# Kernel tuning notes

Hardware: AMD Instinct MI355X
Metric: run time of the kernel (lower is better)

Reference implementation:

```python
import jax, jax.numpy as jnp
import numpy as np

B, S, DIN, DOUT, R, NL, T = 4, 4096, 1024, 1024, 16, 8, 4

def setup_inputs() -> dict:
    key = jax.random.key(0)
    k1, k2, k3, k4, k5 = jax.random.split(key, 5)
    return {
        "x": jax.random.normal(k1, (B, S, DIN), dtype=jnp.float32),
        "W": jax.random.normal(k2, (DOUT, DIN), dtype=jnp.float32) * 0.02,
        "bias": jax.random.normal(k3, (DOUT,), dtype=jnp.float32) * 0.02,
        "lora_A": jax.random.normal(k4, (NL, R, DIN), dtype=jnp.float32) * 0.02,
        "lora_B": jax.random.normal(k5, (NL, DOUT, R), dtype=jnp.float32) * 0.02,
        "tuner_index": jnp.arange(T, dtype=jnp.int64) if jax.config.jax_enable_x64 else jnp.arange(T, dtype=jnp.int32),
    }

def reference(x, W, bias, lora_A, lora_B, tuner_index):
    # Per adapter ti: F.linear(x, W + B_ti @ A_ti, bias)
    # == x @ W.T + (x @ A_ti.T) @ B_ti.T + bias  (fused low-rank form, same math)
    A = lora_A[tuner_index]   # [T, r, Din]
    Bm = lora_B[tuner_index]  # [T, Dout, r]
    base = jnp.einsum('bsd,od->bso', x, W) + bias          # [B, S, Dout]
    low = jnp.einsum('bsd,trd->tbsr', x, A)                # [T, B, S, r]
    delta = jnp.einsum('tbsr,tor->tbso', low, Bm)          # [T, B, S, Dout]
    return base[None, ...] + delta                         # [T, B, S, Dout]
```

## Files before the change

kernel.cpp:

```cpp
#include <hip/hip_runtime.h>


typedef __attribute__((ext_vector_type(8))) _Float16 f16x8;
typedef __attribute__((ext_vector_type(4))) float f32x4;
typedef __attribute__((ext_vector_type(4))) unsigned short us4;
typedef __attribute__((ext_vector_type(8))) unsigned short us8;

namespace {
constexpr int kM = 16384, kDin = 1024, kDout = 1024, kR = 16, kT = 4;
constexpr size_t OFF_XF  = 0;
constexpr size_t OFF_WF  = 33554432;
constexpr size_t OFF_LOW = 35651584;
}

__device__ inline unsigned short f2h(float f) {
  _Float16 h = (_Float16)f;
  return __builtin_bit_cast(unsigned short, h);
}
__device__ inline void gload_lds16(const void* g, void* l) {
  __builtin_amdgcn_global_load_lds(
      (const __attribute__((address_space(1))) unsigned int*)g,
      (__attribute__((address_space(3))) unsigned int*)l, 16, 0, 0);
}
__device__ inline f32x4 mfma_f16(f16x8 a, f16x8 b, f32x4 c) {
  return __builtin_amdgcn_mfma_f32_16x16x32_f16(a, b, c, 0, 0, 0);
}

__global__ __launch_bounds__(256) void cvt_W(const float* __restrict__ W,
                                             unsigned short* __restrict__ wf) {
  constexpr int NW4 = kDout * kDin / 4;
  const int stride = gridDim.x * blockDim.x;
  for (int j = blockIdx.x * blockDim.x + threadIdx.x; j < NW4; j += stride) {
    const float4 v = ((const float4*)W)[j];
    us4 h;
    h[0] = f2h(v.x); h[1] = f2h(v.y); h[2] = f2h(v.z); h[3] = f2h(v.w);
    ((us4*)wf)[j] = h;
  }
}

__global__ __launch_bounds__(256) void lora_low(const float* __restrict__ x,
                                                const float* __restrict__ A,
                                                const int* __restrict__ tuner,
                                                unsigned short* __restrict__ lowb,
                                                unsigned short* __restrict__ xf) {
  __shared__ float xs[64][34];
  __shared__ float as[64][66];
  const int tid = threadIdx.x;
  const int i0  = blockIdx.x * 32;
  const int tx  = tid & 15;
  const int ty  = tid >> 4;
  float acc[2][4] = {{0.f, 0.f, 0.f, 0.f}, {0.f, 0.f, 0.f, 0.f}};

  for (int kt = 0; kt < kDin; kt += 64) {
    __syncthreads();
#pragma unroll
    for (int p = 0; p < 2; ++p) {
      const int f = tid + p * 256;
      const int row = f >> 4, kq = (f & 15) * 4;
      const float4 v = *(const float4*)(x + (size_t)(i0 + row) * kDin + kt + kq);
      xs[kq + 0][row] = v.x; xs[kq + 1][row] = v.y;
      xs[kq + 2][row] = v.z; xs[kq + 3][row] = v.w;
      us4 h;
      h[0] = f2h(v.x); h[1] = f2h(v.y); h[2] = f2h(v.z); h[3] = f2h(v.w);
      *(us4*)(xf + (size_t)(i0 + row) * kDin + kt + kq) = h;
    }
#pragma unroll
    for (int p = 0; p < 4; ++p) {
      const int f = tid + p * 256;
      const int ar = f >> 4, kq = (f & 15) * 4;
      const int ti = tuner[ar >> 4];
      const float4 v = *(const float4*)(A + ((size_t)ti * kR + (ar & 15)) * kDin + kt + kq);
      as[kq + 0][ar] = v.x; as[kq + 1][ar] = v.y;
      as[kq + 2][ar] = v.z; as[kq + 3][ar] = v.w;
    }
    __syncthreads();
#pragma unroll 8
    for (int k = 0; k < 64; ++k) {
      const float a0 = xs[k][ty * 2], a1 = xs[k][ty * 2 + 1];
      const float b0 = as[k][tx * 4], b1 = as[k][tx * 4 + 1];
      const float b2 = as[k][tx * 4 + 2], b3 = as[k][tx * 4 + 3];
      acc[0][0] += a0 * b0; acc[0][1] += a0 * b1; acc[0][2] += a0 * b2; acc[0][3] += a0 * b3;
      acc[1][0] += a1 * b0; acc[1][1] += a1 * b1; acc[1][2] += a1 * b2; acc[1][3] += a1 * b3;
    }
  }
#pragma unroll
  for (int ii = 0; ii < 2; ++ii) {
    us4 o;
#pragma unroll
    for (int j = 0; j < 4; ++j) o[j] = f2h(acc[ii][j]);
    *(us4*)(lowb + ((size_t)(tx >> 2) * kM + i0 + ty * 2 + ii) * kR + (tx & 3) * 4) = o;
  }
}

__global__ __launch_bounds__(256) void lora_main(
    const unsigned short* __restrict__ xf, const unsigned short* __restrict__ wf,
    const float* __restrict__ bias, const float* __restrict__ Bm,
    const int* __restrict__ tuner, const unsigned short* __restrict__ lowb,
    float* __restrict__ out) {
  __shared__ __align__(16) unsigned char smem[32768];
  const int tid  = threadIdx.x;
  const int lane = tid & 63;
  const int w    = tid >> 6;

  const int swz = ((int)blockIdx.x & 7) * 128 + ((int)blockIdx.x >> 3);
  const int bm = swz >> 3, bn = swz & 7;
  const size_t i0 = (size_t)bm * 128, j0 = (size_t)bn * 128;
  const int wm = w >> 1, wn = w & 1;

  const int wp = w & 1;
  const unsigned short* gsrc = (w < 2) ? xf : wf;
  const size_t grow0 = ((w < 2) ? i0 : j0) + wp * 64;
  const unsigned short* gbase =
      gsrc + (grow0 + (lane >> 2)) * kDin + ((lane & 3) ^ ((lane >> 3) & 3)) * 8;
  const int stoff = (w >> 1) * 8192 + wp * 4096;

  f32x4 acc[4][4];
#pragma unroll
  for (int n = 0; n < 4; ++n)
#pragma unroll
    for (int m = 0; m < 4; ++m) acc[n][m] = (f32x4){0.f, 0.f, 0.f, 0.f};

  const int kg = lane >> 4;
  const int rl = lane & 15;
  const int csw = kg ^ ((rl >> 1) & 3);
  const int rdA = (wm * 64 + rl) * 64 + csw * 16;
  const int rdB = 8192 + (wn * 64 + rl) * 64 + csw * 16;

  auto compute_step = [&](const unsigned char* B0) {
    f16x8 a[4], b[4];
#pragma unroll
    for (int m = 0; m < 4; ++m) {
      a[m] = *(const f16x8*)(B0 + rdA + m * 1024);
      b[m] = *(const f16x8*)(B0 + rdB + m * 1024);
    }
    __builtin_amdgcn_s_setprio(1);
#pragma unroll
    for (int n = 0; n < 4; ++n)
#pragma unroll
      for (int m = 0; m < 4; ++m)
        acc[n][m] = mfma_f16(b[n], a[m], acc[n][m]);
    __builtin_amdgcn_s_setprio(0);
  };

  {
    unsigned char* dst = smem + stoff;
#pragma unroll
    for (int c = 0; c < 4; ++c)
      gload_lds16(gbase + c * 16 * kDin, dst + c * 1024);
  }

  for (int s = 0; s < 31; ++s) {
    const int p = s & 1;
    {
      unsigned char* dst = smem + (p ^ 1) * 16384 + stoff;
      const unsigned short* src = gbase + (s + 1) * 32;
#pragma unroll
      for (int c = 0; c < 4; ++c)
        gload_lds16(src + c * 16 * kDin, dst + c * 1024);
    }
    asm volatile("s_waitcnt vmcnt(4)" ::: "memory");
    __builtin_amdgcn_s_barrier();
    asm volatile("" ::: "memory");
    compute_step(smem + p * 16384);
    asm volatile("s_waitcnt lgkmcnt(0)" ::: "memory");
    __builtin_amdgcn_s_barrier();
    asm volatile("" ::: "memory");
  }
  asm volatile("s_waitcnt vmcnt(0)" ::: "memory");
  __builtin_amdgcn_s_barrier();
  asm volatile("" ::: "memory");
  compute_step(smem + 16384);

#pragma unroll
  for (int n = 0; n < 4; ++n) {
    const f32x4 bv = *(const f32x4*)(bias + j0 + wn * 64 + n * 16 + kg * 4);
#pragma unroll
    for (int m = 0; m < 4; ++m)
#pragma unroll
      for (int r = 0; r < 4; ++r) acc[n][m][r] += bv[r];
  }

  {
    unsigned char* p = (tid < 128) ? (smem + 4096 + tid * 32)
                                   : (smem + 12288 + (tid - 128) * 32);
    const us8 z = {0, 0, 0, 0, 0, 0, 0, 0};
    *(us8*)p = z;
    *(us8*)(p + 16) = z;
  }

  for (int t = 0; t < kT; ++t) {
    __syncthreads();
    {
      const int row = tid >> 1, half = tid & 1;
      const us8 lv = *(const us8*)(lowb + ((size_t)t * kM + i0 + row) * kR + half * 8);
      *(us8*)(smem + half * 2048 + row * 16) = lv;
      const int ti = tuner[t];
      const float* bp = Bm + ((size_t)ti * kDout + j0 + row) * kR + half * 8;
      const float4 m0 = *(const float4*)bp;
      const float4 m1 = *(const float4*)(bp + 4);
      us8 mv;
      mv[0] = f2h(m0.x); mv[1] = f2h(m0.y); mv[2] = f2h(m0.z); mv[3] = f2h(m0.w);
      mv[4] = f2h(m1.x); mv[5] = f2h(m1.y); mv[6] = f2h(m1.z); mv[7] = f2h(m1.w);
      *(us8*)(smem + 8192 + half * 2048 + row * 16) = mv;
    }
    __syncthreads();

    f16x8 lf[4], mf[4];
#pragma unroll
    for (int m = 0; m < 4; ++m)
      lf[m] = *(const f16x8*)(smem + kg * 2048 + (wm * 64 + m * 16 + rl) * 16);
#pragma unroll
    for (int n = 0; n < 4; ++n)
      mf[n] = *(const f16x8*)(smem + 8192 + kg * 2048 + (wn * 64 + n * 16 + rl) * 16);

#pragma unroll
    for (int n = 0; n < 4; ++n)
#pragma unroll
      for (int m = 0; m < 4; ++m) {
        const f32x4 d = mfma_f16(mf[n], lf[m], acc[n][m]);
        const size_t row = (size_t)t * kM + i0 + wm * 64 + m * 16 + rl;
        const int    col = (int)j0 + wn * 64 + n * 16 + kg * 4;
        *(f32x4*)(out + row * kDout + col) = d;
      }
  }
}

extern "C" void kernel_launch(void* const* d_in, const int* in_sizes, int n_in,
                              void* d_out, int out_size, void* d_ws, size_t ws_size,
                              hipStream_t stream) {
  const float* x    = (const float*)d_in[0];
  const float* W    = (const float*)d_in[1];
  const float* bias = (const float*)d_in[2];
  const float* lA   = (const float*)d_in[3];
  const float* lB   = (const float*)d_in[4];
  const int*   ti   = (const int*)d_in[5];
  float* out = (float*)d_out;

  unsigned char* ws = (unsigned char*)d_ws;
  unsigned short* xfp  = (unsigned short*)(ws + OFF_XF);
  unsigned short* wfp  = (unsigned short*)(ws + OFF_WF);
  unsigned short* lowb = (unsigned short*)(ws + OFF_LOW);

  cvt_W<<<64, 256, 0, stream>>>(W, wfp);
  lora_low<<<kM / 32, 256, 0, stream>>>(x, lA, ti, lowb, xfp);
  lora_main<<<1024, 256, 0, stream>>>(xfp, wfp, bias, lB, ti, lowb, out);
}
```

Before: 170.6 us.

## Fuse W conversion into lora_low, shrink main tile to 128x64, nontemporal stores

```diff
diff --git a/kernel.cpp b/kernel.cpp
--- a/kernel.cpp
+++ b/kernel.cpp
@@ -26,23 +26,25 @@
   return __builtin_amdgcn_mfma_f32_16x16x32_f16(a, b, c, 0, 0, 0);
 }
 
-__global__ __launch_bounds__(256) void cvt_W(const float* __restrict__ W,
-                                             unsigned short* __restrict__ wf) {
-  constexpr int NW4 = kDout * kDin / 4;
-  const int stride = gridDim.x * blockDim.x;
-  for (int j = blockIdx.x * blockDim.x + threadIdx.x; j < NW4; j += stride) {
-    const float4 v = ((const float4*)W)[j];
-    us4 h;
-    h[0] = f2h(v.x); h[1] = f2h(v.y); h[2] = f2h(v.z); h[3] = f2h(v.w);
-    ((us4*)wf)[j] = h;
-  }
-}
-
 __global__ __launch_bounds__(256) void lora_low(const float* __restrict__ x,
+                                                const float* __restrict__ W,
                                                 const float* __restrict__ A,
                                                 const int* __restrict__ tuner,
                                                 unsigned short* __restrict__ lowb,
-                                                unsigned short* __restrict__ xf) {
+                                                unsigned short* __restrict__ xf,
+                                                unsigned short* __restrict__ wf) {
+  {
+    const int idx = blockIdx.x * 256 + threadIdx.x;
+#pragma unroll
+    for (int p = 0; p < 2; ++p) {
+      const int j = idx + p * 131072;
+      const float4 v = ((const float4*)W)[j];
+      us4 h;
+      h[0] = f2h(v.x); h[1] = f2h(v.y); h[2] = f2h(v.z); h[3] = f2h(v.w);
+      ((us4*)wf)[j] = h;
+    }
+  }
+
   __shared__ float xs[64][34];
   __shared__ float as[64][66];
   const int tid = threadIdx.x;
@@ -97,26 +99,31 @@
     const float* __restrict__ bias, const float* __restrict__ Bm,
     const int* __restrict__ tuner, const unsigned short* __restrict__ lowb,
     float* __restrict__ out) {
-  __shared__ __align__(16) unsigned char smem[32768];
+  __shared__ __align__(16) unsigned char smem[24576];
   const int tid  = threadIdx.x;
   const int lane = tid & 63;
   const int w    = tid >> 6;
 
-  const int swz = ((int)blockIdx.x & 7) * 128 + ((int)blockIdx.x >> 3);
-  const int bm = swz >> 3, bn = swz & 7;
-  const size_t i0 = (size_t)bm * 128, j0 = (size_t)bn * 128;
+  const int swz = ((int)blockIdx.x & 7) * 256 + ((int)blockIdx.x >> 3);
+  const int bm = swz >> 4, bn = swz & 15;
+  const size_t i0 = (size_t)bm * 128, j0 = (size_t)bn * 64;
   const int wm = w >> 1, wn = w & 1;
 
-  const int wp = w & 1;
-  const unsigned short* gsrc = (w < 2) ? xf : wf;
-  const size_t grow0 = ((w < 2) ? i0 : j0) + wp * 64;
-  const unsigned short* gbase =
-      gsrc + (grow0 + (lane >> 2)) * kDin + ((lane & 3) ^ ((lane >> 3) & 3)) * 8;
-  const int stoff = (w >> 1) * 8192 + wp * 4096;
-
-  f32x4 acc[4][4];
-#pragma unroll
-  for (int n = 0; n < 4; ++n)
+  const int chsw = ((lane & 3) ^ ((lane >> 3) & 3)) * 8;
+  const unsigned short* gsrc_q[3];
+  int ldsoff_q[3];
+#pragma unroll
+  for (int q = 0; q < 3; ++q) {
+    const int c = 3 * w + q;
+    const bool isA = c < 8;
+    const size_t rowb = (isA ? i0 + c * 16 : j0 + (c - 8) * 16) + (lane >> 2);
+    gsrc_q[q] = (isA ? xf : wf) + rowb * kDin + chsw;
+    ldsoff_q[q] = c * 1024;
+  }
+
+  f32x4 acc[2][4];
+#pragma unroll
+  for (int n = 0; n < 2; ++n)
 #pragma unroll
     for (int m = 0; m < 4; ++m) acc[n][m] = (f32x4){0.f, 0.f, 0.f, 0.f};
 
@@ -124,44 +131,40 @@
   const int rl = lane & 15;
   const int csw = kg ^ ((rl >> 1) & 3);
   const int rdA = (wm * 64 + rl) * 64 + csw * 16;
-  const int rdB = 8192 + (wn * 64 + rl) * 64 + csw * 16;
+  const int rdB = 8192 + (wn * 32 + rl) * 64 + csw * 16;
 
   auto compute_step = [&](const unsigned char* B0) {
-    f16x8 a[4], b[4];
-#pragma unroll
-    for (int m = 0; m < 4; ++m) {
-      a[m] = *(const f16x8*)(B0 + rdA + m * 1024);
-      b[m] = *(const f16x8*)(B0 + rdB + m * 1024);
-    }
+    f16x8 a[4], b[2];
+#pragma unroll
+    for (int m = 0; m < 4; ++m) a[m] = *(const f16x8*)(B0 + rdA + m * 1024);
+#pragma unroll
+    for (int n = 0; n < 2; ++n) b[n] = *(const f16x8*)(B0 + rdB + n * 1024);
     __builtin_amdgcn_s_setprio(1);
 #pragma unroll
-    for (int n = 0; n < 4; ++n)
+    for (int n = 0; n < 2; ++n)
 #pragma unroll
       for (int m = 0; m < 4; ++m)
         acc[n][m] = mfma_f16(b[n], a[m], acc[n][m]);
     __builtin_amdgcn_s_setprio(0);
   };
 
-  {
-    unsigned char* dst = smem + stoff;
-#pragma unroll
-    for (int c = 0; c < 4; ++c)
-      gload_lds16(gbase + c * 16 * kDin, dst + c * 1024);
-  }
+#pragma unroll
+  for (int q = 0; q < 3; ++q)
+    gload_lds16(gsrc_q[q], smem + ldsoff_q[q]);
 
   for (int s = 0; s < 31; ++s) {
     const int p = s & 1;
     {
-      unsigned char* dst = smem + (p ^ 1) * 16384 + stoff;
-      const unsigned short* src = gbase + (s + 1) * 32;
-#pragma unroll
-      for (int c = 0; c < 4; ++c)
-        gload_lds16(src + c * 16 * kDin, dst + c * 1024);
-    }
-    asm volatile("s_waitcnt vmcnt(4)" ::: "memory");
+      unsigned char* dst = smem + (p ^ 1) * 12288;
+      const int ko = (s + 1) * 32;
+#pragma unroll
+      for (int q = 0; q < 3; ++q)
+        gload_lds16(gsrc_q[q] + ko, dst + ldsoff_q[q]);
+    }
+    asm volatile("s_waitcnt vmcnt(3)" ::: "memory");
     __builtin_amdgcn_s_barrier();
     asm volatile("" ::: "memory");
-    compute_step(smem + p * 16384);
+    compute_step(smem + p * 12288);
     asm volatile("s_waitcnt lgkmcnt(0)" ::: "memory");
     __builtin_amdgcn_s_barrier();
     asm volatile("" ::: "memory");
@@ -169,11 +172,11 @@
   asm volatile("s_waitcnt vmcnt(0)" ::: "memory");
   __builtin_amdgcn_s_barrier();
   asm volatile("" ::: "memory");
-  compute_step(smem + 16384);
-
-#pragma unroll
-  for (int n = 0; n < 4; ++n) {
-    const f32x4 bv = *(const f32x4*)(bias + j0 + wn * 64 + n * 16 + kg * 4);
+  compute_step(smem + 12288);
+
+#pragma unroll
+  for (int n = 0; n < 2; ++n) {
+    const f32x4 bv = *(const f32x4*)(bias + j0 + wn * 32 + n * 16 + kg * 4);
 #pragma unroll
     for (int m = 0; m < 4; ++m)
 #pragma unroll
@@ -181,11 +184,15 @@
   }
 
   {
-    unsigned char* p = (tid < 128) ? (smem + 4096 + tid * 32)
-                                   : (smem + 12288 + (tid - 128) * 32);
-    const us8 z = {0, 0, 0, 0, 0, 0, 0, 0};
-    *(us8*)p = z;
-    *(us8*)(p + 16) = z;
+    if (tid < 128) {
+      const us8 z = {0, 0, 0, 0, 0, 0, 0, 0};
+      *(us8*)(smem + 4096 + tid * 32) = z;
+      *(us8*)(smem + 4096 + tid * 32 + 16) = z;
+    } else if (tid < 192) {
+      const us8 z = {0, 0, 0, 0, 0, 0, 0, 0};
+      *(us8*)(smem + 10240 + (tid - 128) * 32) = z;
+      *(us8*)(smem + 10240 + (tid - 128) * 32 + 16) = z;
+    }
   }
 
   for (int t = 0; t < kT; ++t) {
@@ -194,33 +201,35 @@
       const int row = tid >> 1, half = tid & 1;
       const us8 lv = *(const us8*)(lowb + ((size_t)t * kM + i0 + row) * kR + half * 8);
       *(us8*)(smem + half * 2048 + row * 16) = lv;
-      const int ti = tuner[t];
-      const float* bp = Bm + ((size_t)ti * kDout + j0 + row) * kR + half * 8;
-      const float4 m0 = *(const float4*)bp;
-      const float4 m1 = *(const float4*)(bp + 4);
-      us8 mv;
-      mv[0] = f2h(m0.x); mv[1] = f2h(m0.y); mv[2] = f2h(m0.z); mv[3] = f2h(m0.w);
-      mv[4] = f2h(m1.x); mv[5] = f2h(m1.y); mv[6] = f2h(m1.z); mv[7] = f2h(m1.w);
-      *(us8*)(smem + 8192 + half * 2048 + row * 16) = mv;
-    }
-    __syncthreads();
-
-    f16x8 lf[4], mf[4];
+      if (tid < 128) {
+        const int ti = tuner[t];
+        const float* bp = Bm + ((size_t)ti * kDout + j0 + row) * kR + half * 8;
+        const float4 m0 = *(const float4*)bp;
+        const float4 m1 = *(const float4*)(bp + 4);
+        us8 mv;
+        mv[0] = f2h(m0.x); mv[1] = f2h(m0.y); mv[2] = f2h(m0.z); mv[3] = f2h(m0.w);
+        mv[4] = f2h(m1.x); mv[5] = f2h(m1.y); mv[6] = f2h(m1.z); mv[7] = f2h(m1.w);
+        *(us8*)(smem + 8192 + half * 1024 + row * 16) = mv;
+      }
+    }
+    __syncthreads();
+
+    f16x8 lf[4], mf[2];
 #pragma unroll
     for (int m = 0; m < 4; ++m)
       lf[m] = *(const f16x8*)(smem + kg * 2048 + (wm * 64 + m * 16 + rl) * 16);
 #pragma unroll
-    for (int n = 0; n < 4; ++n)
-      mf[n] = *(const f16x8*)(smem + 8192 + kg * 2048 + (wn * 64 + n * 16 + rl) * 16);
-
-#pragma unroll
-    for (int n = 0; n < 4; ++n)
+    for (int n = 0; n < 2; ++n)
+      mf[n] = *(const f16x8*)(smem + 8192 + kg * 1024 + (wn * 32 + n * 16 + rl) * 16);
+
+#pragma unroll
+    for (int n = 0; n < 2; ++n)
 #pragma unroll
       for (int m = 0; m < 4; ++m) {
         const f32x4 d = mfma_f16(mf[n], lf[m], acc[n][m]);
         const size_t row = (size_t)t * kM + i0 + wm * 64 + m * 16 + rl;
-        const int    col = (int)j0 + wn * 64 + n * 16 + kg * 4;
-        *(f32x4*)(out + row * kDout + col) = d;
+        const int    col = (int)j0 + wn * 32 + n * 16 + kg * 4;
+        __builtin_nontemporal_store(d, (f32x4*)(out + row * kDout + col));
       }
   }
 }
@@ -241,7 +250,6 @@
   unsigned short* wfp  = (unsigned short*)(ws + OFF_WF);
   unsigned short* lowb = (unsigned short*)(ws + OFF_LOW);
 
-  cvt_W<<<64, 256, 0, stream>>>(W, wfp);
-  lora_low<<<kM / 32, 256, 0, stream>>>(x, lA, ti, lowb, xfp);
-  lora_main<<<1024, 256, 0, stream>>>(xfp, wfp, bias, lB, ti, lowb, out);
-}
+  lora_low<<<kM / 32, 256, 0, stream>>>(x, W, lA, ti, lowb, xfp, wfp);
+  lora_main<<<2048, 256, 0, stream>>>(xfp, wfp, bias, lB, ti, lowb, out);
+}
```

Result: faster. 159.6 us (-6.5%).
